# Kernel optimization log

Hardware: AMD Instinct MI355X
Metric: run time of the kernel (lower is better)

Reference implementation:

```python
import jax, jax.numpy as jnp
import numpy as np

B = 512          # batch of trees
L = 2048         # leaves per tree (perfect binary tree)
VOCAB = 100000
D_IN = 128       # input_dim
H = 128          # hidden_dim
NUM_CLASSES = 2


def setup_inputs() -> dict:
    key = jax.random.key(0)
    ks = jax.random.split(key, 8)
    leaf_ids = jax.random.randint(ks[0], (B, L), 0, VOCAB)
    # learned params (xavier-ish scales; exact init values don't matter for the baseline)
    embedding = jax.random.normal(ks[1], (VOCAB, D_IN), dtype=jnp.float32) * 0.1
    W_in = jax.random.normal(ks[2], (D_IN, H), dtype=jnp.float32) * (1.0 / np.sqrt(D_IN))
    b_in = jnp.zeros((H,), dtype=jnp.float32)
    W_comp = jax.random.normal(ks[3], (2 * H, H), dtype=jnp.float32) * (1.0 / np.sqrt(2 * H))
    b_comp = jnp.zeros((H,), dtype=jnp.float32)
    W_cls = jax.random.normal(ks[4], (H, NUM_CLASSES), dtype=jnp.float32) * (1.0 / np.sqrt(H))
    b_cls = jnp.zeros((NUM_CLASSES,), dtype=jnp.float32)
    return {"leaf_ids": leaf_ids, "embedding": embedding, "W_in": W_in, "b_in": b_in,
            "W_comp": W_comp, "b_comp": b_comp, "W_cls": W_cls, "b_cls": b_cls}


def reference(leaf_ids, embedding, W_in, b_in, W_comp, b_comp, W_cls, b_cls):
    # Leaves: embedding gather -> input_projection (dropout is identity in eval)
    h = embedding[leaf_ids] @ W_in + b_in            # [B, L, H]
    # Depth-batched binary composition up the perfect binary tree:
    # torch.cat([left, right]) @ composition -> tanh, level by level.
    n = L
    while n > 1:
        pairs = h.reshape(B, n // 2, 2 * H)          # contiguous (left, right) concat
        h = jnp.tanh(pairs @ W_comp + b_comp)        # [B, n//2, H]
        n //= 2
    root = h[:, 0]                                   # [B, H]
    return root @ W_cls + b_cls                      # [B, NUM_CLASSES]
```

## Files before the change

kernel.cpp:

```cpp
#include <hip/hip_runtime.h>

typedef __attribute__((ext_vector_type(8))) short s16x8;
typedef __attribute__((ext_vector_type(4))) float f32x4;

#define BB   512
#define LL   2048
#define DD   128
#define HH   128
#define SUB  128
#define NSUB (LL / SUB)
#define K1ROWS 8
#define K2ROWS (NSUB * K1ROWS)

__device__ __forceinline__ short f2bf(float x) {
  unsigned u = __builtin_bit_cast(unsigned, x);
  u += 0x7fffu + ((u >> 16) & 1u);
  return (short)(u >> 16);
}
__device__ __forceinline__ unsigned pk_bf16(float a, float b) {
  unsigned r;
  asm("v_cvt_pk_bf16_f32 %0, %1, %2" : "=v"(r) : "v"(a), "v"(b));
  return r;
}
__device__ __forceinline__ float tanh_fast(float x) {
  float e2 = __expf(2.f * x);
  return (e2 - 1.f) * __builtin_amdgcn_rcpf(e2 + 1.f);
}

__device__ __forceinline__ int swz(int row, int inner) {
  return row * 256 + (inner ^ (((row >> 1) & 7) << 4));
}

__global__ __launch_bounds__(256) void k_prep(
    const float* __restrict__ Win, const float* __restrict__ Wcomp,
    short* __restrict__ WiT, short* __restrict__ WcT) {
  const int i0 = blockIdx.x * 256 + threadIdx.x;
  const int stride = gridDim.x * 256;
  for (int idx = i0; idx < 128 * 128; idx += stride) {
    int n = idx >> 7, k = idx & 127;
    WiT[idx] = f2bf(Win[k * 128 + n]);
  }
  for (int idx = i0; idx < 128 * 256; idx += stride) {
    int n = idx >> 8, k = idx & 255;
    WcT[idx] = f2bf(Wcomp[k * 128 + n]);
  }
}

__device__ __forceinline__ void tree_mm(const short* src, int mt_in,
                                        const s16x8 (&wfc)[8][2], int lm,
                                        int lh, f32x4& c0, f32x4& c1) {
  s16x8 a[8];
#pragma unroll
  for (int kt = 0; kt < 8; ++kt) {
    int k = kt * 32 + lh * 8;
    int rowbuf = 2 * (mt_in * 16 + lm) + (k >> 7);
    a[kt] = *(const s16x8*)((const char*)src + swz(rowbuf, (k & 127) * 2));
  }
  c0 = (f32x4){0.f, 0.f, 0.f, 0.f};
  c1 = (f32x4){0.f, 0.f, 0.f, 0.f};
#pragma unroll
  for (int kt = 0; kt < 8; ++kt) {
    c0 = __builtin_amdgcn_mfma_f32_16x16x32_bf16(a[kt], wfc[kt][0], c0, 0, 0, 0);
    c1 = __builtin_amdgcn_mfma_f32_16x16x32_bf16(a[kt], wfc[kt][1], c1, 0, 0, 0);
  }
}

__device__ __forceinline__ void h0_tile(const short* ldsE, short* ldsB,
                                        int mtl, int mtg,
                                        const s16x8 (&wfin)[4][2], float bi0,
                                        float bi1, int lm, int lh, int col0) {
  s16x8 a[4];
#pragma unroll
  for (int kt = 0; kt < 4; ++kt)
    a[kt] = *(const s16x8*)((const char*)ldsE +
                            swz(mtl * 16 + lm, kt * 64 + lh * 16));
  f32x4 c0 = {0.f, 0.f, 0.f, 0.f}, c1 = {0.f, 0.f, 0.f, 0.f};
#pragma unroll
  for (int kt = 0; kt < 4; ++kt) {
    c0 = __builtin_amdgcn_mfma_f32_16x16x32_bf16(a[kt], wfin[kt][0], c0, 0, 0, 0);
    c1 = __builtin_amdgcn_mfma_f32_16x16x32_bf16(a[kt], wfin[kt][1], c1, 0, 0, 0);
  }
#pragma unroll
  for (int r = 0; r < 4; ++r) {
    int row = mtg * 16 + lh * 4 + r;
    *(unsigned*)((char*)ldsB + swz(row, col0 * 2)) =
        pk_bf16(c0[r] + bi0, c1[r] + bi1);
  }
}

__global__ __launch_bounds__(256, 3) void k_subtree(
    const int* __restrict__ ids, const float* __restrict__ emb,
    const short* __restrict__ WiT, const float* __restrict__ bin,
    const short* __restrict__ WcT, const float* __restrict__ bcomp,
    short* __restrict__ wsbf) {
  __shared__ __align__(16) short ldsE[64 * 128];
  __shared__ __align__(16) short ldsB[128 * 128];
  const int blk = blockIdx.x, tid = threadIdx.x;
  const int wave = tid >> 6, lane = tid & 63;
  const int lh = lane >> 4, lm = lane & 15;
  const int n0 = wave * 32;
  const int col0 = n0 + 2 * lm;

  int idv[16];
#pragma unroll
  for (int it = 0; it < 16; ++it)
    idv[it] = ids[(long)blk * SUB + it * 8 + wave * 2 + (lane >> 5)];

  s16x8 wfin[4][2];
#pragma unroll
  for (int kt = 0; kt < 4; ++kt)
#pragma unroll
    for (int nt = 0; nt < 2; ++nt)
      wfin[kt][nt] = *(const s16x8*)(WiT + (col0 + nt) * 128 + kt * 32 + lh * 8);
  const float2 biv = *(const float2*)(bin + col0);
  const float2 bcv = *(const float2*)(bcomp + col0);

#pragma unroll
  for (int it = 0; it < 8; ++it) {
    int r = it * 8 + wave * 2 + (lane >> 5);
    const float4 v = ((const float4*)(emb + (long)idv[it] * DD))[lane & 31];
    uint2 pv;
    pv.x = pk_bf16(v.x, v.y);
    pv.y = pk_bf16(v.z, v.w);
    *(uint2*)((char*)ldsE + swz(r, (lane & 31) * 8)) = pv;
  }
  float4 g1[8];
#pragma unroll
  for (int j = 0; j < 8; ++j)
    g1[j] = ((const float4*)(emb + (long)idv[8 + j] * DD))[lane & 31];
  __syncthreads();

#pragma unroll 1
  for (int mtl = 0; mtl < 4; ++mtl)
    h0_tile(ldsE, ldsB, mtl, mtl, wfin, biv.x, biv.y, lm, lh, col0);
  __syncthreads();

#pragma unroll
  for (int j = 0; j < 8; ++j) {
    int r = j * 8 + wave * 2 + (lane >> 5);
    uint2 pv;
    pv.x = pk_bf16(g1[j].x, g1[j].y);
    pv.y = pk_bf16(g1[j].z, g1[j].w);
    *(uint2*)((char*)ldsE + swz(r, (lane & 31) * 8)) = pv;
  }
  __syncthreads();

#pragma unroll 1
  for (int mtl = 0; mtl < 4; ++mtl)
    h0_tile(ldsE, ldsB, mtl, 4 + mtl, wfin, biv.x, biv.y, lm, lh, col0);

  s16x8 wfc[8][2];
#pragma unroll
  for (int kt = 0; kt < 8; ++kt)
#pragma unroll
    for (int nt = 0; nt < 2; ++nt)
      wfc[kt][nt] = *(const s16x8*)(WcT + (col0 + nt) * 256 + kt * 32 + lh * 8);
  __syncthreads();

#pragma unroll 1
  for (int mt = 0; mt < 4; ++mt) {
    f32x4 c0, c1;
    tree_mm(ldsB, mt, wfc, lm, lh, c0, c1);
#pragma unroll
    for (int r = 0; r < 4; ++r) {
      int row = mt * 16 + lh * 4 + r;
      *(unsigned*)((char*)ldsE + swz(row, col0 * 2)) =
          pk_bf16(tanh_fast(c0[r] + bcv.x), tanh_fast(c1[r] + bcv.y));
    }
  }
  __syncthreads();

#pragma unroll 1
  for (int mt = 0; mt < 2; ++mt) {
    f32x4 c0, c1;
    tree_mm(ldsE, mt, wfc, lm, lh, c0, c1);
#pragma unroll
    for (int r = 0; r < 4; ++r) {
      int row = mt * 16 + lh * 4 + r;
      *(unsigned*)((char*)ldsB + swz(row, col0 * 2)) =
          pk_bf16(tanh_fast(c0[r] + bcv.x), tanh_fast(c1[r] + bcv.y));
    }
  }
  __syncthreads();

  {
    f32x4 c0, c1;
    tree_mm(ldsB, 0, wfc, lm, lh, c0, c1);
#pragma unroll
    for (int r = 0; r < 4; ++r) {
      int row = lh * 4 + r;
      *(unsigned*)((char*)ldsE + swz(row, col0 * 2)) =
          pk_bf16(tanh_fast(c0[r] + bcv.x), tanh_fast(c1[r] + bcv.y));
    }
  }
  __syncthreads();

  {
    f32x4 c0, c1;
    tree_mm(ldsE, 0, wfc, lm, lh, c0, c1);
#pragma unroll
    for (int r = 0; r < 4; ++r) {
      int row = lh * 4 + r;
      if (row < K1ROWS)
        *(unsigned*)(wsbf + ((long)blk * K1ROWS + row) * HH + col0) =
            pk_bf16(tanh_fast(c0[r] + bcv.x), tanh_fast(c1[r] + bcv.y));
    }
  }
}

__global__ __launch_bounds__(256, 2) void k_tree2(
    const short* __restrict__ wsbf, const short* __restrict__ WcT,
    const float* __restrict__ bcomp, const float* __restrict__ Wcls,
    const float* __restrict__ bcls, float* __restrict__ out) {
  __shared__ __align__(16) short srcL[128 * 128];
  __shared__ __align__(16) short dstS[64 * 128];
  __shared__ float rootL[128];
  const int b = blockIdx.x, tid = threadIdx.x;
  const int wave = tid >> 6, lane = tid & 63;
  const int lh = lane >> 4, lm = lane & 15;
  const int n0 = wave * 32;
  const int col0 = n0 + 2 * lm;

  s16x8 wfc[8][2];
#pragma unroll
  for (int kt = 0; kt < 8; ++kt)
#pragma unroll
    for (int nt = 0; nt < 2; ++nt)
      wfc[kt][nt] = *(const s16x8*)(WcT + (col0 + nt) * 256 + kt * 32 + lh * 8);
  const float2 bcv = *(const float2*)(bcomp + col0);

#pragma unroll
  for (int it = 0; it < 8; ++it) {
    int row = it * 16 + (tid >> 4);
    s16x8 v = *(const s16x8*)(wsbf + ((long)b * K2ROWS + row) * HH + (tid & 15) * 8);
    *(s16x8*)((char*)srcL + swz(row, (tid & 15) * 16)) = v;
  }
  __syncthreads();

  const short* src = srcL;
  short* dst = dstS;
  const int mtiles[7] = {4, 2, 1, 1, 1, 1, 1};
  const int rlim[7] = {64, 32, 16, 8, 4, 2, 1};
#pragma unroll 1
  for (int lev = 0; lev < 7; ++lev) {
    int nmt = mtiles[lev], rl = rlim[lev];
#pragma unroll 1
    for (int mt = 0; mt < nmt; ++mt) {
      f32x4 c0, c1;
      tree_mm(src, mt, wfc, lm, lh, c0, c1);
      if (lev == 6) {
        if (lh == 0) {
          rootL[col0] = tanh_fast(c0[0] + bcv.x);
          rootL[col0 + 1] = tanh_fast(c1[0] + bcv.y);
        }
      } else {
#pragma unroll
        for (int r = 0; r < 4; ++r) {
          int row = mt * 16 + lh * 4 + r;
          if (row < rl)
            *(unsigned*)((char*)dst + swz(row, col0 * 2)) =
                pk_bf16(tanh_fast(c0[r] + bcv.x), tanh_fast(c1[r] + bcv.y));
        }
      }
    }
    __syncthreads();
    const short* t = src;
    src = dst;
    dst = (short*)t;
  }

  if (wave == 0) {
    int c = lane & 1, kb = lane >> 1;
    float p = 0.f;
#pragma unroll
    for (int j = 0; j < 4; ++j) {
      int k = kb + 32 * j;
      p += rootL[k] * Wcls[k * 2 + c];
    }
#pragma unroll
    for (int m = 2; m <= 32; m <<= 1) p += __shfl_xor(p, m, 64);
    if (lane < 2) out[b * 2 + lane] = p + bcls[lane];
  }
}

extern "C" void kernel_launch(void* const* d_in, const int* in_sizes, int n_in,
                              void* d_out, int out_size, void* d_ws, size_t ws_size,
                              hipStream_t stream) {
  const int*   ids   = (const int*)d_in[0];
  const float* emb   = (const float*)d_in[1];
  const float* Win   = (const float*)d_in[2];
  const float* bin   = (const float*)d_in[3];
  const float* Wcomp = (const float*)d_in[4];
  const float* bcomp = (const float*)d_in[5];
  const float* Wcls  = (const float*)d_in[6];
  const float* bcls  = (const float*)d_in[7];
  char* wsb = (char*)d_ws;
  short* wsbf = (short*)wsb;
  const size_t WSBF_BYTES = (size_t)BB * NSUB * K1ROWS * HH * 2;
  short* WcT = (short*)(wsb + WSBF_BYTES);
  short* WiT = (short*)(wsb + WSBF_BYTES + 65536);
  float* out = (float*)d_out;

  hipLaunchKernelGGL(k_prep, dim3(64), dim3(256), 0, stream, Win, Wcomp, WiT, WcT);
  hipLaunchKernelGGL(k_subtree, dim3(BB * NSUB), dim3(256), 0, stream,
                     ids, emb, WiT, bin, WcT, bcomp, wsbf);
  hipLaunchKernelGGL(k_tree2, dim3(BB), dim3(256), 0, stream,
                     wsbf, WcT, bcomp, Wcls, bcls, out);
}
```

Measured before the change: 161.7 us.

## Halve per-block subtree size to raise occupancy and block count

Each block now processes 64-leaf subtrees instead of 128, which doubles the number of blocks. It halves the ldsB buffer, drops the two-phase embedding gather and the h0_tile helper, and raises launch bounds to 5 blocks per CU. The goal is more latency hiding for the gather-bound first stage through higher occupancy. The cost is that the second kernel must reduce twice as many subtree roots, and the per-block work is lower relative to the fixed cost of loading weights into registers.

Result: slower. 227.1 us (+40.4%).

```diff
diff --git a/kernel.cpp b/kernel.cpp
--- a/kernel.cpp
+++ b/kernel.cpp
@@ -7,9 +7,9 @@
 #define LL   2048
 #define DD   128
 #define HH   128
-#define SUB  128
+#define SUB  64
 #define NSUB (LL / SUB)
-#define K1ROWS 8
+#define K1ROWS 4
 #define K2ROWS (NSUB * K1ROWS)
 
 __device__ __forceinline__ short f2bf(float x) {
@@ -65,46 +65,23 @@
   }
 }
 
-__device__ __forceinline__ void h0_tile(const short* ldsE, short* ldsB,
-                                        int mtl, int mtg,
-                                        const s16x8 (&wfin)[4][2], float bi0,
-                                        float bi1, int lm, int lh, int col0) {
-  s16x8 a[4];
-#pragma unroll
-  for (int kt = 0; kt < 4; ++kt)
-    a[kt] = *(const s16x8*)((const char*)ldsE +
-                            swz(mtl * 16 + lm, kt * 64 + lh * 16));
-  f32x4 c0 = {0.f, 0.f, 0.f, 0.f}, c1 = {0.f, 0.f, 0.f, 0.f};
-#pragma unroll
-  for (int kt = 0; kt < 4; ++kt) {
-    c0 = __builtin_amdgcn_mfma_f32_16x16x32_bf16(a[kt], wfin[kt][0], c0, 0, 0, 0);
-    c1 = __builtin_amdgcn_mfma_f32_16x16x32_bf16(a[kt], wfin[kt][1], c1, 0, 0, 0);
-  }
-#pragma unroll
-  for (int r = 0; r < 4; ++r) {
-    int row = mtg * 16 + lh * 4 + r;
-    *(unsigned*)((char*)ldsB + swz(row, col0 * 2)) =
-        pk_bf16(c0[r] + bi0, c1[r] + bi1);
-  }
-}
-
-__global__ __launch_bounds__(256, 3) void k_subtree(
+__global__ __launch_bounds__(256, 5) void k_subtree(
     const int* __restrict__ ids, const float* __restrict__ emb,
     const short* __restrict__ WiT, const float* __restrict__ bin,
     const short* __restrict__ WcT, const float* __restrict__ bcomp,
     short* __restrict__ wsbf) {
   __shared__ __align__(16) short ldsE[64 * 128];
-  __shared__ __align__(16) short ldsB[128 * 128];
+  __shared__ __align__(16) short ldsB[64 * 128];
   const int blk = blockIdx.x, tid = threadIdx.x;
   const int wave = tid >> 6, lane = tid & 63;
   const int lh = lane >> 4, lm = lane & 15;
   const int n0 = wave * 32;
   const int col0 = n0 + 2 * lm;
 
-  int idv[16];
-#pragma unroll
-  for (int it = 0; it < 16; ++it)
-    idv[it] = ids[(long)blk * SUB + it * 8 + wave * 2 + (lane >> 5)];
+  int idv[8];
+#pragma unroll
+  for (int it = 0; it < 8; ++it)
+    idv[it] = ids[(long)blk * SUB + it * 8 + (tid >> 5)];
 
   s16x8 wfin[4][2];
 #pragma unroll
@@ -117,37 +94,35 @@
 
 #pragma unroll
   for (int it = 0; it < 8; ++it) {
-    int r = it * 8 + wave * 2 + (lane >> 5);
-    const float4 v = ((const float4*)(emb + (long)idv[it] * DD))[lane & 31];
+    int r = it * 8 + (tid >> 5);
+    const float4 v = ((const float4*)(emb + (long)idv[it] * DD))[tid & 31];
     uint2 pv;
     pv.x = pk_bf16(v.x, v.y);
     pv.y = pk_bf16(v.z, v.w);
-    *(uint2*)((char*)ldsE + swz(r, (lane & 31) * 8)) = pv;
-  }
-  float4 g1[8];
-#pragma unroll
-  for (int j = 0; j < 8; ++j)
-    g1[j] = ((const float4*)(emb + (long)idv[8 + j] * DD))[lane & 31];
-  __syncthreads();
-
-#pragma unroll 1
-  for (int mtl = 0; mtl < 4; ++mtl)
-    h0_tile(ldsE, ldsB, mtl, mtl, wfin, biv.x, biv.y, lm, lh, col0);
-  __syncthreads();
-
-#pragma unroll
-  for (int j = 0; j < 8; ++j) {
-    int r = j * 8 + wave * 2 + (lane >> 5);
-    uint2 pv;
-    pv.x = pk_bf16(g1[j].x, g1[j].y);
-    pv.y = pk_bf16(g1[j].z, g1[j].w);
-    *(uint2*)((char*)ldsE + swz(r, (lane & 31) * 8)) = pv;
-  }
-  __syncthreads();
-
-#pragma unroll 1
-  for (int mtl = 0; mtl < 4; ++mtl)
-    h0_tile(ldsE, ldsB, mtl, 4 + mtl, wfin, biv.x, biv.y, lm, lh, col0);
+    *(uint2*)((char*)ldsE + swz(r, (tid & 31) * 8)) = pv;
+  }
+  __syncthreads();
+
+#pragma unroll 1
+  for (int mt = 0; mt < 4; ++mt) {
+    s16x8 a[4];
+#pragma unroll
+    for (int kt = 0; kt < 4; ++kt)
+      a[kt] = *(const s16x8*)((const char*)ldsE +
+                              swz(mt * 16 + lm, kt * 64 + lh * 16));
+    f32x4 c0 = {0.f, 0.f, 0.f, 0.f}, c1 = {0.f, 0.f, 0.f, 0.f};
+#pragma unroll
+    for (int kt = 0; kt < 4; ++kt) {
+      c0 = __builtin_amdgcn_mfma_f32_16x16x32_bf16(a[kt], wfin[kt][0], c0, 0, 0, 0);
+      c1 = __builtin_amdgcn_mfma_f32_16x16x32_bf16(a[kt], wfin[kt][1], c1, 0, 0, 0);
+    }
+#pragma unroll
+    for (int r = 0; r < 4; ++r) {
+      int row = mt * 16 + lh * 4 + r;
+      *(unsigned*)((char*)ldsB + swz(row, col0 * 2)) =
+          pk_bf16(c0[r] + biv.x, c1[r] + biv.y);
+    }
+  }
 
   s16x8 wfc[8][2];
 #pragma unroll
@@ -158,7 +133,7 @@
   __syncthreads();
 
 #pragma unroll 1
-  for (int mt = 0; mt < 4; ++mt) {
+  for (int mt = 0; mt < 2; ++mt) {
     f32x4 c0, c1;
     tree_mm(ldsB, mt, wfc, lm, lh, c0, c1);
 #pragma unroll
@@ -170,13 +145,12 @@
   }
   __syncthreads();
 
-#pragma unroll 1
-  for (int mt = 0; mt < 2; ++mt) {
-    f32x4 c0, c1;
-    tree_mm(ldsE, mt, wfc, lm, lh, c0, c1);
-#pragma unroll
-    for (int r = 0; r < 4; ++r) {
-      int row = mt * 16 + lh * 4 + r;
+  {
+    f32x4 c0, c1;
+    tree_mm(ldsE, 0, wfc, lm, lh, c0, c1);
+#pragma unroll
+    for (int r = 0; r < 4; ++r) {
+      int row = lh * 4 + r;
       *(unsigned*)((char*)ldsB + swz(row, col0 * 2)) =
           pk_bf16(tanh_fast(c0[r] + bcv.x), tanh_fast(c1[r] + bcv.y));
     }
```

## Make subtree kernel persistent and prefetch next subtree's embeddings during compute

Applied to the files above, without the earlier changes.

Converts k_subtree from one block per subtree (8192 blocks) into a persistent grid of 768 blocks that loop over subtrees. Composition weights are loaded into registers once per block, and the ids and first-half embedding gathers for the next subtree are issued during the current subtree's tree reduction. The aim is to hide gather latency and cut per-block setup costs. In exchange, register pressure rises: wfin is reloaded every iteration and extra prefetch buffers are live. That could reduce occupancy under launch_bounds(256,3).

Result: slower. 229.6 us (+42.0%).

```diff
diff --git a/kernel.cpp b/kernel.cpp
--- a/kernel.cpp
+++ b/kernel.cpp
@@ -9,6 +9,8 @@
 #define HH   128
 #define SUB  128
 #define NSUB (LL / SUB)
+#define NBLK (BB * NSUB)
+#define GRID 768
 #define K1ROWS 8
 #define K2ROWS (NSUB * K1ROWS)
 
@@ -95,116 +97,140 @@
     short* __restrict__ wsbf) {
   __shared__ __align__(16) short ldsE[64 * 128];
   __shared__ __align__(16) short ldsB[128 * 128];
-  const int blk = blockIdx.x, tid = threadIdx.x;
+  const int tid = threadIdx.x;
   const int wave = tid >> 6, lane = tid & 63;
   const int lh = lane >> 4, lm = lane & 15;
   const int n0 = wave * 32;
   const int col0 = n0 + 2 * lm;
-
-  int idv[16];
-#pragma unroll
-  for (int it = 0; it < 16; ++it)
-    idv[it] = ids[(long)blk * SUB + it * 8 + wave * 2 + (lane >> 5)];
-
-  s16x8 wfin[4][2];
-#pragma unroll
-  for (int kt = 0; kt < 4; ++kt)
+  const int gr = tid >> 5;
+  const int gc = tid & 31;
+
+  s16x8 wfc[8][2];
+#pragma unroll
+  for (int kt = 0; kt < 8; ++kt)
 #pragma unroll
     for (int nt = 0; nt < 2; ++nt)
-      wfin[kt][nt] = *(const s16x8*)(WiT + (col0 + nt) * 128 + kt * 32 + lh * 8);
+      wfc[kt][nt] = *(const s16x8*)(WcT + (col0 + nt) * 256 + kt * 32 + lh * 8);
   const float2 biv = *(const float2*)(bin + col0);
   const float2 bcv = *(const float2*)(bcomp + col0);
 
-#pragma unroll
-  for (int it = 0; it < 8; ++it) {
-    int r = it * 8 + wave * 2 + (lane >> 5);
-    const float4 v = ((const float4*)(emb + (long)idv[it] * DD))[lane & 31];
-    uint2 pv;
-    pv.x = pk_bf16(v.x, v.y);
-    pv.y = pk_bf16(v.z, v.w);
-    *(uint2*)((char*)ldsE + swz(r, (lane & 31) * 8)) = pv;
-  }
-  float4 g1[8];
-#pragma unroll
-  for (int j = 0; j < 8; ++j)
-    g1[j] = ((const float4*)(emb + (long)idv[8 + j] * DD))[lane & 31];
-  __syncthreads();
-
-#pragma unroll 1
-  for (int mtl = 0; mtl < 4; ++mtl)
-    h0_tile(ldsE, ldsB, mtl, mtl, wfin, biv.x, biv.y, lm, lh, col0);
-  __syncthreads();
-
+  int idv[16];
+#pragma unroll
+  for (int it = 0; it < 16; ++it)
+    idv[it] = ids[(long)blockIdx.x * SUB + it * 8 + gr];
+  uint2 gp0[8];
 #pragma unroll
   for (int j = 0; j < 8; ++j) {
-    int r = j * 8 + wave * 2 + (lane >> 5);
-    uint2 pv;
-    pv.x = pk_bf16(g1[j].x, g1[j].y);
-    pv.y = pk_bf16(g1[j].z, g1[j].w);
-    *(uint2*)((char*)ldsE + swz(r, (lane & 31) * 8)) = pv;
-  }
-  __syncthreads();
-
-#pragma unroll 1
-  for (int mtl = 0; mtl < 4; ++mtl)
-    h0_tile(ldsE, ldsB, mtl, 4 + mtl, wfin, biv.x, biv.y, lm, lh, col0);
-
-  s16x8 wfc[8][2];
-#pragma unroll
-  for (int kt = 0; kt < 8; ++kt)
-#pragma unroll
-    for (int nt = 0; nt < 2; ++nt)
-      wfc[kt][nt] = *(const s16x8*)(WcT + (col0 + nt) * 256 + kt * 32 + lh * 8);
-  __syncthreads();
-
-#pragma unroll 1
-  for (int mt = 0; mt < 4; ++mt) {
-    f32x4 c0, c1;
-    tree_mm(ldsB, mt, wfc, lm, lh, c0, c1);
-#pragma unroll
-    for (int r = 0; r < 4; ++r) {
-      int row = mt * 16 + lh * 4 + r;
-      *(unsigned*)((char*)ldsE + swz(row, col0 * 2)) =
-          pk_bf16(tanh_fast(c0[r] + bcv.x), tanh_fast(c1[r] + bcv.y));
-    }
-  }
-  __syncthreads();
-
-#pragma unroll 1
-  for (int mt = 0; mt < 2; ++mt) {
-    f32x4 c0, c1;
-    tree_mm(ldsE, mt, wfc, lm, lh, c0, c1);
-#pragma unroll
-    for (int r = 0; r < 4; ++r) {
-      int row = mt * 16 + lh * 4 + r;
-      *(unsigned*)((char*)ldsB + swz(row, col0 * 2)) =
-          pk_bf16(tanh_fast(c0[r] + bcv.x), tanh_fast(c1[r] + bcv.y));
-    }
-  }
-  __syncthreads();
-
-  {
-    f32x4 c0, c1;
-    tree_mm(ldsB, 0, wfc, lm, lh, c0, c1);
-#pragma unroll
-    for (int r = 0; r < 4; ++r) {
-      int row = lh * 4 + r;
-      *(unsigned*)((char*)ldsE + swz(row, col0 * 2)) =
-          pk_bf16(tanh_fast(c0[r] + bcv.x), tanh_fast(c1[r] + bcv.y));
-    }
-  }
-  __syncthreads();
-
-  {
-    f32x4 c0, c1;
-    tree_mm(ldsE, 0, wfc, lm, lh, c0, c1);
-#pragma unroll
-    for (int r = 0; r < 4; ++r) {
-      int row = lh * 4 + r;
-      if (row < K1ROWS)
-        *(unsigned*)(wsbf + ((long)blk * K1ROWS + row) * HH + col0) =
+    const float4 v = ((const float4*)(emb + (long)idv[j] * DD))[gc];
+    gp0[j].x = pk_bf16(v.x, v.y);
+    gp0[j].y = pk_bf16(v.z, v.w);
+  }
+
+#pragma unroll 1
+  for (int s = blockIdx.x; s < NBLK; s += GRID) {
+#pragma unroll
+    for (int j = 0; j < 8; ++j)
+      *(uint2*)((char*)ldsE + swz(j * 8 + gr, gc * 8)) = gp0[j];
+    s16x8 wfin[4][2];
+#pragma unroll
+    for (int kt = 0; kt < 4; ++kt)
+#pragma unroll
+      for (int nt = 0; nt < 2; ++nt)
+        wfin[kt][nt] =
+            *(const s16x8*)(WiT + (col0 + nt) * 128 + kt * 32 + lh * 8);
+    __syncthreads();
+
+    float4 g1[8];
+#pragma unroll
+    for (int j = 0; j < 8; ++j)
+      g1[j] = ((const float4*)(emb + (long)idv[8 + j] * DD))[gc];
+
+#pragma unroll 1
+    for (int mtl = 0; mtl < 4; ++mtl)
+      h0_tile(ldsE, ldsB, mtl, mtl, wfin, biv.x, biv.y, lm, lh, col0);
+    __syncthreads();
+
+#pragma unroll
+    for (int j = 0; j < 8; ++j) {
+      uint2 pv;
+      pv.x = pk_bf16(g1[j].x, g1[j].y);
+      pv.y = pk_bf16(g1[j].z, g1[j].w);
+      *(uint2*)((char*)ldsE + swz(j * 8 + gr, gc * 8)) = pv;
+    }
+    {
+      int sn = s + GRID;
+      if (sn >= NBLK) sn = 0;
+#pragma unroll
+      for (int it = 0; it < 16; ++it)
+        idv[it] = ids[(long)sn * SUB + it * 8 + gr];
+    }
+    __syncthreads();
+
+#pragma unroll 1
+    for (int mtl = 0; mtl < 4; ++mtl)
+      h0_tile(ldsE, ldsB, mtl, 4 + mtl, wfin, biv.x, biv.y, lm, lh, col0);
+
+    float4 gn[8];
+#pragma unroll
+    for (int j = 0; j < 8; ++j)
+      gn[j] = ((const float4*)(emb + (long)idv[j] * DD))[gc];
+    __syncthreads();
+
+#pragma unroll 1
+    for (int mt = 0; mt < 4; ++mt) {
+      f32x4 c0, c1;
+      tree_mm(ldsB, mt, wfc, lm, lh, c0, c1);
+#pragma unroll
+      for (int r = 0; r < 4; ++r) {
+        int row = mt * 16 + lh * 4 + r;
+        *(unsigned*)((char*)ldsE + swz(row, col0 * 2)) =
             pk_bf16(tanh_fast(c0[r] + bcv.x), tanh_fast(c1[r] + bcv.y));
-    }
+      }
+    }
+#pragma unroll
+    for (int j = 0; j < 8; ++j) {
+      gp0[j].x = pk_bf16(gn[j].x, gn[j].y);
+      gp0[j].y = pk_bf16(gn[j].z, gn[j].w);
+    }
+    __syncthreads();
+
+#pragma unroll 1
+    for (int mt = 0; mt < 2; ++mt) {
+      f32x4 c0, c1;
+      tree_mm(ldsE, mt, wfc, lm, lh, c0, c1);
+#pragma unroll
+      for (int r = 0; r < 4; ++r) {
+        int row = mt * 16 + lh * 4 + r;
+        *(unsigned*)((char*)ldsB + swz(row, col0 * 2)) =
+            pk_bf16(tanh_fast(c0[r] + bcv.x), tanh_fast(c1[r] + bcv.y));
+      }
+    }
+    __syncthreads();
+
+    {
+      f32x4 c0, c1;
+      tree_mm(ldsB, 0, wfc, lm, lh, c0, c1);
+#pragma unroll
+      for (int r = 0; r < 4; ++r) {
+        int row = lh * 4 + r;
+        *(unsigned*)((char*)ldsE + swz(row, col0 * 2)) =
+            pk_bf16(tanh_fast(c0[r] + bcv.x), tanh_fast(c1[r] + bcv.y));
+      }
+    }
+    __syncthreads();
+
+    {
+      f32x4 c0, c1;
+      tree_mm(ldsE, 0, wfc, lm, lh, c0, c1);
+#pragma unroll
+      for (int r = 0; r < 4; ++r) {
+        int row = lh * 4 + r;
+        if (row < K1ROWS)
+          *(unsigned*)(wsbf + ((long)s * K1ROWS + row) * HH + col0) =
+              pk_bf16(tanh_fast(c0[r] + bcv.x), tanh_fast(c1[r] + bcv.y));
+      }
+    }
+    __syncthreads();
   }
 }
 
@@ -302,7 +328,7 @@
   float* out = (float*)d_out;
 
   hipLaunchKernelGGL(k_prep, dim3(64), dim3(256), 0, stream, Win, Wcomp, WiT, WcT);
-  hipLaunchKernelGGL(k_subtree, dim3(BB * NSUB), dim3(256), 0, stream,
+  hipLaunchKernelGGL(k_subtree, dim3(GRID), dim3(256), 0, stream,
                      ids, emb, WiT, bin, WcT, bcomp, wsbf);
   hipLaunchKernelGGL(k_tree2, dim3(BB), dim3(256), 0, stream,
                      wsbf, WcT, bcomp, Wcls, bcls, out);
```
